# Kernel tuning notes

Measured on AMD Instinct MI355X. Metric: run time of the kernel, lower is better.

Reference implementation:

```python
import jax, jax.numpy as jnp
import numpy as np

N_NODES = 100000
N_EDGES = 1600000
NUM_FEATURES = 32
EDGE_DIM = 8
GAT_DIM = 16
HEADS = 4
HID = GAT_DIM * HEADS  # 64
OUT_DIM = 2
NUM_GRAPHS = 64
NEG_SLOPE = 0.2


def setup_inputs() -> dict:
    key = jax.random.key(0)
    ks = jax.random.split(key, 24)
    g = lambda k, shp, fan: jax.random.normal(k, shp, jnp.float32) * (1.0 / np.sqrt(fan))
    inp = {
        'x': jax.random.normal(ks[0], (N_NODES, NUM_FEATURES), jnp.float32),
        'edge_index': jax.random.randint(ks[1], (2, N_EDGES), 0, N_NODES, jnp.int64),
        'edge_attr': jax.random.normal(ks[2], (N_EDGES, EDGE_DIM), jnp.float32),
        'batch': jnp.sort(jax.random.randint(ks[3], (N_NODES,), 0, NUM_GRAPHS, jnp.int64)),
        # input GATConv params (PyG: lin bias-free, att_* of shape [H,C], bias [H*C])
        'W0': g(ks[4], (NUM_FEATURES, HID), NUM_FEATURES),
        'att_src0': g(ks[5], (HEADS, GAT_DIM), GAT_DIM),
        'att_dst0': g(ks[6], (HEADS, GAT_DIM), GAT_DIM),
        'We0': g(ks[7], (EDGE_DIM, HID), EDGE_DIM),
        'att_e0': g(ks[8], (HEADS, GAT_DIM), GAT_DIM),
        'b0': jnp.zeros((HID,), jnp.float32),
        # 2 hidden GATConv layers, stacked on a leading layer axis
        'Wh': g(ks[9], (2, HID, HID), HID),
        'att_src_h': g(ks[10], (2, HEADS, GAT_DIM), GAT_DIM),
        'att_dst_h': g(ks[11], (2, HEADS, GAT_DIM), GAT_DIM),
        'We_h': g(ks[12], (2, EDGE_DIM, HID), EDGE_DIM),
        'att_e_h': g(ks[13], (2, HEADS, GAT_DIM), GAT_DIM),
        'bh': jnp.zeros((2, HID), jnp.float32),
        # MLP head
        'fc1_w': g(ks[14], (HID, 2 * GAT_DIM), HID),
        'fc1_b': jnp.zeros((2 * GAT_DIM,), jnp.float32),
        'fc2_w': g(ks[15], (2 * GAT_DIM, OUT_DIM), 2 * GAT_DIM),
        'fc2_b': jnp.zeros((OUT_DIM,), jnp.float32),
    }
    return inp


def _gat_conv(x, src, dst, ea, W, a_s, a_d, We, a_e, b, n_nodes):
    # x: [N, Fin] -> out: [N, H*C]
    xp = (x @ W).reshape(n_nodes, HEADS, GAT_DIM)
    al_s = jnp.einsum('nhc,hc->nh', xp, a_s)            # per-node src logits
    al_d = jnp.einsum('nhc,hc->nh', xp, a_d)
    ep = (ea @ We).reshape(-1, HEADS, GAT_DIM)
    al_e = jnp.einsum('ehc,hc->eh', ep, a_e)
    alpha = jax.nn.leaky_relu(al_s[src] + al_d[dst] + al_e, NEG_SLOPE)  # [E,H]
    m = jax.ops.segment_max(alpha, dst, num_segments=n_nodes)
    m = jnp.where(jnp.isfinite(m), m, 0.0)              # nodes with no in-edges
    ex = jnp.exp(alpha - m[dst])
    den = jax.ops.segment_sum(ex, dst, num_segments=n_nodes)
    coef = ex / (den[dst] + 1e-16)                      # segment softmax over dst
    out = jax.ops.segment_sum(xp[src] * coef[..., None], dst, num_segments=n_nodes)
    return out.reshape(n_nodes, HID) + b


def _forward(x, edge_index, edge_attr, batch, W0, att_src0, att_dst0, We0, att_e0,
             b0, Wh, att_src_h, att_dst_h, We_h, att_e_h, bh, fc1_w, fc1_b, fc2_w, fc2_b):
    n = x.shape[0]
    src, dst = edge_index[0], edge_index[1]
    # PyG add_self_loops(fill_value='mean'): self-loop attr = mean of incoming edge attrs
    cnt = jax.ops.segment_sum(jnp.ones((src.shape[0],), x.dtype), dst, num_segments=n)
    mean_attr = jax.ops.segment_sum(edge_attr, dst, num_segments=n) / jnp.clip(cnt, 1.0)[:, None]
    loop = jnp.arange(n, dtype=src.dtype)
    src_sl = jnp.concatenate([src, loop])
    dst_sl = jnp.concatenate([dst, loop])
    ea_sl = jnp.concatenate([edge_attr, mean_attr], axis=0)

    h = _gat_conv(x, src_sl, dst_sl, ea_sl, W0, att_src0, att_dst0, We0, att_e0, b0, n)
    h = jax.nn.relu(h)
    for i in range(2):  # source has `x - F.relu(x)` (no-op): no ReLU between hidden layers
        h = _gat_conv(h, src_sl, dst_sl, ea_sl, Wh[i], att_src_h[i], att_dst_h[i],
                      We_h[i], att_e_h[i], bh[i], n)
    # global_mean_pool over graphs
    ones = jnp.ones((n,), h.dtype)
    gcnt = jax.ops.segment_sum(ones, batch, num_segments=NUM_GRAPHS)
    pooled = jax.ops.segment_sum(h, batch, num_segments=NUM_GRAPHS) / jnp.clip(gcnt, 1.0)[:, None]
    y = jax.nn.relu(pooled @ fc1_w + fc1_b)
    return y @ fc2_w + fc2_b


def reference(x, edge_index, edge_attr, batch, W0, att_src0, att_dst0, We0, att_e0,
              b0, Wh, att_src_h, att_dst_h, We_h, att_e_h, bh, fc1_w, fc1_b, fc2_w, fc2_b):
    return _forward(x, edge_index, edge_attr, batch, W0, att_src0, att_dst0, We0, att_e0,
                    b0, Wh, att_src_h, att_dst_h, We_h, att_e_h, bh, fc1_w, fc1_b, fc2_w, fc2_b)
```

## Files before the change

### kernel.cpp

```cpp
#include <hip/hip_runtime.h>
#include <hip/hip_bf16.h>
#include <hip/hip_fp16.h>

#define N_NODES 100000
#define N_EDGES 1600000
#define HID 64
#define NUM_GRAPHS 64
#define NEG_SLOPE 0.2f
#define SCAN_CHUNK 1024
#define SCAN_NB ((N_NODES + SCAN_CHUNK - 1) / SCAN_CHUNK)
#define ROW_W 8
#define XP_NODES_PER_BLK 16
#define POOL_NODES_PER_BLK 256
#define BUILD_NB (N_EDGES / 128)
#define XP0_NB (N_NODES / 16)


__global__ void hist_kernel(const int* __restrict__ ei, int* __restrict__ cnt,
                            int* __restrict__ rank) {
    int e = blockIdx.x * blockDim.x + threadIdx.x;
    if (e >= N_EDGES) return;
    rank[e] = atomicAdd(&cnt[ei[N_EDGES + e]], 1);
}

__global__ void scan_local_kernel(const int* __restrict__ cnt, int* __restrict__ row_ptr,
                                  int* __restrict__ bsum) {
    __shared__ int s[256];
    int t = threadIdx.x;
    int base = blockIdx.x * SCAN_CHUNK + t * 4;
    int v[4]; int sum = 0;
    #pragma unroll
    for (int i = 0; i < 4; ++i) {
        int idx = base + i;
        v[i] = (idx < N_NODES) ? cnt[idx] : 0;
        sum += v[i];
    }
    s[t] = sum;
    __syncthreads();
    for (int off = 1; off < 256; off <<= 1) {
        int x = (t >= off) ? s[t - off] : 0;
        __syncthreads();
        s[t] += x;
        __syncthreads();
    }
    int run = s[t] - sum;
    #pragma unroll
    for (int i = 0; i < 4; ++i) {
        int idx = base + i;
        if (idx < N_NODES) row_ptr[idx] = run;
        run += v[i];
    }
    if (t == 255) bsum[blockIdx.x] = s[255];
}

__global__ void scan_bsum_kernel(int* __restrict__ bsum) {
    int t = threadIdx.x;
    int orig = (t < SCAN_NB) ? bsum[t] : 0;
    int v = orig;
    #pragma unroll
    for (int off = 1; off < 64; off <<= 1) {
        int u = __shfl_up(v, off);
        if ((t & 63) >= off) v += u;
    }
    __shared__ int wtot;
    if (t == 63) wtot = v;
    __syncthreads();
    if (t >= 64) v += wtot;
    if (t < SCAN_NB) bsum[t] = v - orig;
}

__global__ void scan_add_kernel(int* __restrict__ row_ptr, const int* __restrict__ bsum) {
    int i = blockIdx.x * blockDim.x + threadIdx.x;
    if (i > N_NODES) return;
    if (i == N_NODES) row_ptr[i] = N_EDGES;
    else row_ptr[i] += bsum[i >> 10];
}

__global__ void weff_all_kernel(const float* __restrict__ We0, const float* __restrict__ ae0,
                                const float* __restrict__ Weh, const float* __restrict__ aeh,
                                float* __restrict__ weff) {
    int t = threadIdx.x;
    if (t >= 96) return;
    int layer = t >> 5, r = t & 31;
    int dd = r >> 2, h = r & 3;
    const float* We = (layer == 0) ? We0 : Weh + (size_t)(layer - 1) * 8 * 64;
    const float* ae = (layer == 0) ? ae0 : aeh + (size_t)(layer - 1) * 64;
    float s = 0.f;
    #pragma unroll
    for (int c = 0; c < 16; ++c) s += We[dd * 64 + h * 16 + c] * ae[h * 16 + c];
    weff[layer * 32 + dd * 4 + h] = s;
}

__global__ __launch_bounds__(256) void build_xp0_kernel(
    const int* __restrict__ ei, const float* __restrict__ ea,
    const int* __restrict__ row_ptr, const int* __restrict__ rank,
    const float* __restrict__ weff, unsigned int* __restrict__ ale_csr,
    const float* __restrict__ x, const float* __restrict__ W0,
    const float* __restrict__ a_s, const float* __restrict__ a_d,
    __half* __restrict__ xp, float* __restrict__ als, float* __restrict__ ald) {
    int b = blockIdx.x;
    int g = b / 3, r3 = b - g * 3;
    if (r3 == 2) {
        int wave = threadIdx.x >> 6, lane = threadIdx.x & 63;
        float wcol[32];
        #pragma unroll
        for (int k = 0; k < 32; ++k) wcol[k] = W0[k * 64 + lane];
        float asl = a_s[lane], adl = a_d[lane];
        int n0 = g * XP_NODES_PER_BLK + wave * 4;
        #pragma unroll 2
        for (int ni = 0; ni < 4; ++ni) {
            int n = n0 + ni;
            const float* xr = x + (size_t)n * 32;
            float a0 = 0.f, a1 = 0.f, a2 = 0.f, a3 = 0.f;
            #pragma unroll
            for (int k = 0; k < 32; k += 4) {
                float4 xv = *(const float4*)(xr + k);
                a0 += xv.x * wcol[k];     a1 += xv.y * wcol[k + 1];
                a2 += xv.z * wcol[k + 2]; a3 += xv.w * wcol[k + 3];
            }
            float acc = (a0 + a1) + (a2 + a3);
            xp[(size_t)n * 64 + lane] = __float2half(acc);
            float ps = acc * asl, pd = acc * adl;
            #pragma unroll
            for (int mk = 8; mk >= 1; mk >>= 1) {
                ps += __shfl_xor(ps, mk, 16);
                pd += __shfl_xor(pd, mk, 16);
            }
            if ((lane & 15) == 0) {
                als[(size_t)n * 4 + (lane >> 4)] = ps;
                ald[(size_t)n * 4 + (lane >> 4)] = pd;
            }
        }
        return;
    }
    int build_b = g * 2 + r3;
    int e = build_b * 128 + (threadIdx.x >> 1);
    int q = threadIdx.x & 1;
    int d = ei[N_EDGES + e];
    float4 a = *((const float4*)(ea + (size_t)e * 8) + q);
    float o0 = __shfl_xor(a.x, 1), o1 = __shfl_xor(a.y, 1);
    float o2 = __shfl_xor(a.z, 1), o3 = __shfl_xor(a.w, 1);
    float av[8];
    av[0] = q ? o0 : a.x;  av[1] = q ? o1 : a.y;
    av[2] = q ? o2 : a.z;  av[3] = q ? o3 : a.w;
    av[4] = q ? a.x : o0;  av[5] = q ? a.y : o1;
    av[6] = q ? a.z : o2;  av[7] = q ? a.w : o3;
    unsigned int w[4];
    if (q == 0) {
        float al[8];
        #pragma unroll
        for (int l = 0; l < 2; ++l) {
            #pragma unroll
            for (int h = 0; h < 4; ++h) {
                float s = 0.f;
                #pragma unroll
                for (int j = 0; j < 8; ++j) s += av[j] * weff[l * 32 + j * 4 + h];
                al[l * 4 + h] = s;
            }
        }
        __half2 p0 = __floats2half2_rn(al[0], al[1]);
        __half2 p1 = __floats2half2_rn(al[2], al[3]);
        __half2 p2 = __floats2half2_rn(al[4], al[5]);
        __half2 p3 = __floats2half2_rn(al[6], al[7]);
        w[0] = *(unsigned int*)&p0; w[1] = *(unsigned int*)&p1;
        w[2] = *(unsigned int*)&p2; w[3] = *(unsigned int*)&p3;
    } else {
        float al[4];
        #pragma unroll
        for (int h = 0; h < 4; ++h) {
            float s = 0.f;
            #pragma unroll
            for (int j = 0; j < 8; ++j) s += av[j] * weff[64 + j * 4 + h];
            al[h] = s;
        }
        __half2 p0 = __floats2half2_rn(al[0], al[1]);
        __half2 p1 = __floats2half2_rn(al[2], al[3]);
        w[0] = *(unsigned int*)&p0; w[1] = *(unsigned int*)&p1;
        w[2] = (unsigned int)ei[e];
        w[3] = 0u;
    }
    int pos = row_ptr[d] + rank[e];
    *(uint4*)(ale_csr + (size_t)pos * ROW_W + q * 4) =
        make_uint4(w[0], w[1], w[2], w[3]);
}

template <bool FUSE_XP>
__global__ __launch_bounds__(256) void gat_node_kernel(
    const int* __restrict__ row_ptr, const unsigned int* __restrict__ ale_csr,
    const float* __restrict__ als, const float* __restrict__ ald,
    const __half* __restrict__ xp, int layer,
    float* __restrict__ out, const float* __restrict__ bias, int relu_flag,
    const float* __restrict__ Wn, const float* __restrict__ asn,
    const float* __restrict__ adn, __half* __restrict__ xpn,
    float* __restrict__ alsn, float* __restrict__ aldn) {
    __shared__ float exl[4 * 256];
    __shared__ int   coll[4 * 64];
    __shared__ float hrow[4 * 64];
    int wave = threadIdx.x >> 6, lane = threadIdx.x & 63;
    int node = blockIdx.x * 4 + wave;
    if (node >= N_NODES) return;
    int start = row_ptr[node], end = row_ptr[node + 1];
    int deg = end - start;
    int wb = wave * 64, wb4 = wave * 256;
    int cq = lane & 15;
    int eg = lane >> 4;
    int hv = cq >> 2;

    float4 ad4  = *(const float4*)(ald + (size_t)node * 4);
    float4 asn4 = *(const float4*)(als + (size_t)node * 4);

    float4 acc4 = make_float4(0.f, 0.f, 0.f, 0.f);
    float csum = 0.f;
    float sm0 = 0.f, sm1 = 0.f, sm2 = 0.f, sm3 = 0.f;

    for (int base = 0; base < deg; base += 64) {
        int cnt = min(64, deg - base);
        float ex0 = 0.f, ex1 = 0.f, ex2 = 0.f, ex3 = 0.f;
        int s = 0;
        if (lane < cnt) {
            const unsigned int* row = ale_csr + (size_t)(start + base + lane) * ROW_W;
            uint2 alew = *(const uint2*)(row + 2 * layer);
            s = (int)row[6];
            float2 e01 = __half22float2(*(const __half2*)&alew.x);
            float2 e23 = __half22float2(*(const __half2*)&alew.y);
            sm0 += e01.x; sm1 += e01.y; sm2 += e23.x; sm3 += e23.y;
            float4 as4 = *(const float4*)(als + (size_t)s * 4);
            float v0 = as4.x + ad4.x + e01.x;
            float v1 = as4.y + ad4.y + e01.y;
            float v2 = as4.z + ad4.z + e23.x;
            float v3 = as4.w + ad4.w + e23.y;
            ex0 = __expf((v0 >= 0.f) ? v0 : NEG_SLOPE * v0);
            ex1 = __expf((v1 >= 0.f) ? v1 : NEG_SLOPE * v1);
            ex2 = __expf((v2 >= 0.f) ? v2 : NEG_SLOPE * v2);
            ex3 = __expf((v3 >= 0.f) ? v3 : NEG_SLOPE * v3);
        }
        *(float4*)(exl + wb4 + lane * 4) = make_float4(ex0, ex1, ex2, ex3);
        coll[wb + lane] = s;
        const float* exw = exl + wb4 + hv;
        int cntUp = (cnt + 15) & ~15;
        for (int j = eg; j < cntUp; j += 16) {
            int s0 = coll[wb + j],     s1 = coll[wb + j + 4];
            int s2 = coll[wb + j + 8], s3 = coll[wb + j + 12];
            float c0 = exw[(j) * 4],      c1 = exw[(j + 4) * 4];
            float c2 = exw[(j + 8) * 4],  c3 = exw[(j + 12) * 4];
            uint2 x0 = *(const uint2*)(xp + (size_t)s0 * 64 + cq * 4);
            uint2 x1 = *(const uint2*)(xp + (size_t)s1 * 64 + cq * 4);
            uint2 x2 = *(const uint2*)(xp + (size_t)s2 * 64 + cq * 4);
            uint2 x3 = *(const uint2*)(xp + (size_t)s3 * 64 + cq * 4);
            float2 f00 = __half22float2(*(const __half2*)&x0.x);
            float2 f01 = __half22float2(*(const __half2*)&x0.y);
            float2 f10 = __half22float2(*(const __half2*)&x1.x);
            float2 f11 = __half22float2(*(const __half2*)&x1.y);
            float2 f20 = __half22float2(*(const __half2*)&x2.x);
            float2 f21 = __half22float2(*(const __half2*)&x2.y);
            float2 f30 = __half22float2(*(const __half2*)&x3.x);
            float2 f31 = __half22float2(*(const __half2*)&x3.y);
            acc4.x += c0 * f00.x + c1 * f10.x + c2 * f20.x + c3 * f30.x;
            acc4.y += c0 * f00.y + c1 * f10.y + c2 * f20.y + c3 * f30.y;
            acc4.z += c0 * f01.x + c1 * f11.x + c2 * f21.x + c3 * f31.x;
            acc4.w += c0 * f01.y + c1 * f11.y + c2 * f21.y + c3 * f31.y;
            csum   += c0 + c1 + c2 + c3;
        }
    }
    #pragma unroll
    for (int mk = 1; mk < 64; mk <<= 1) {
        sm0 += __shfl_xor(sm0, mk);
        sm1 += __shfl_xor(sm1, mk);
        sm2 += __shfl_xor(sm2, mk);
        sm3 += __shfl_xor(sm3, mk);
    }
    float minv = 1.f / (float)max(deg, 1);
    float sv0 = asn4.x + ad4.x + sm0 * minv;
    float sv1 = asn4.y + ad4.y + sm1 * minv;
    float sv2 = asn4.z + ad4.z + sm2 * minv;
    float sv3 = asn4.w + ad4.w + sm3 * minv;
    float exs0 = __expf((sv0 >= 0.f) ? sv0 : NEG_SLOPE * sv0);
    float exs1 = __expf((sv1 >= 0.f) ? sv1 : NEG_SLOPE * sv1);
    float exs2 = __expf((sv2 >= 0.f) ? sv2 : NEG_SLOPE * sv2);
    float exs3 = __expf((sv3 >= 0.f) ? sv3 : NEG_SLOPE * sv3);
    float exsl = (hv < 2) ? ((hv == 0) ? exs0 : exs1)
                          : ((hv == 2) ? exs2 : exs3);
    if (eg == 0) {
        uint2 xn = *(const uint2*)(xp + (size_t)node * 64 + cq * 4);
        float2 g0 = __half22float2(*(const __half2*)&xn.x);
        float2 g1 = __half22float2(*(const __half2*)&xn.y);
        acc4.x += exsl * g0.x;
        acc4.y += exsl * g0.y;
        acc4.z += exsl * g1.x;
        acc4.w += exsl * g1.y;
        csum   += exsl;
    }
    #pragma unroll
    for (int mk = 16; mk < 64; mk <<= 1) {
        acc4.x += __shfl_xor(acc4.x, mk);
        acc4.y += __shfl_xor(acc4.y, mk);
        acc4.z += __shfl_xor(acc4.z, mk);
        acc4.w += __shfl_xor(acc4.w, mk);
        csum   += __shfl_xor(csum, mk);
    }
    float inv = 1.f / (csum + 1e-16f);
    float4 b4 = *(const float4*)(bias + cq * 4);
    float4 v;
    v.x = acc4.x * inv + b4.x;
    v.y = acc4.y * inv + b4.y;
    v.z = acc4.z * inv + b4.z;
    v.w = acc4.w * inv + b4.w;
    if (relu_flag) {
        v.x = fmaxf(v.x, 0.f); v.y = fmaxf(v.y, 0.f);
        v.z = fmaxf(v.z, 0.f); v.w = fmaxf(v.w, 0.f);
    }
    if (!FUSE_XP) {
        if (eg == 0)
            *(float4*)(out + (size_t)node * 64 + cq * 4) = v;
    } else {
        if (eg == 0) *(float4*)(hrow + wb + cq * 4) = v;
        float acc = 0.f;
        #pragma unroll
        for (int k0 = 0; k0 < 64; k0 += 8) {
            float wv[8];
            #pragma unroll
            for (int j = 0; j < 8; ++j) wv[j] = Wn[(k0 + j) * 64 + lane];
            #pragma unroll
            for (int j = 0; j < 8; ++j) acc += hrow[wb + k0 + j] * wv[j];
        }
        xpn[(size_t)node * 64 + lane] = __float2half(acc);
        float ps = acc * asn[lane], pd = acc * adn[lane];
        #pragma unroll
        for (int mk = 8; mk >= 1; mk >>= 1) {
            ps += __shfl_xor(ps, mk, 16);
            pd += __shfl_xor(pd, mk, 16);
        }
        if ((lane & 15) == 0) {
            alsn[(size_t)node * 4 + (lane >> 4)] = ps;
            aldn[(size_t)node * 4 + (lane >> 4)] = pd;
        }
    }
}

__global__ void pool_kernel(const float* __restrict__ h, const int* __restrict__ batch,
                            float* __restrict__ pooled) {
    int base = blockIdx.x * POOL_NODES_PER_BLK;
    int tid = threadIdx.x;
    int c = tid & 63, r = tid >> 6;
    float acc = 0.f;
    int curg = -1;
    for (int i = r; i < POOL_NODES_PER_BLK; i += 4) {
        int n = base + i;
        if (n >= N_NODES) break;
        int g = batch[n];
        if (g != curg) {
            if (curg >= 0) atomicAdd(&pooled[curg * 64 + c], acc);
            curg = g; acc = 0.f;
        }
        acc += h[(size_t)n * 64 + c];
    }
    if (curg >= 0) atomicAdd(&pooled[curg * 64 + c], acc);
}

__global__ void mlp_kernel(const float* __restrict__ pooled, const int* __restrict__ batch,
                           const float* __restrict__ w1, const float* __restrict__ b1,
                           const float* __restrict__ w2, const float* __restrict__ b2,
                           float* __restrict__ y) {
    int g = blockIdx.x, t = threadIdx.x;
    __shared__ float p[64], f1[32];
    __shared__ float invc_s;
    if (t == 0) {
        int lo = 0, hi = N_NODES;
        while (lo < hi) { int mid = (lo + hi) >> 1; if (batch[mid] < g) lo = mid + 1; else hi = mid; }
        int start = lo;
        hi = N_NODES;
        while (lo < hi) { int mid = (lo + hi) >> 1; if (batch[mid] < g + 1) lo = mid + 1; else hi = mid; }
        invc_s = 1.f / fmaxf((float)(lo - start), 1.f);
    }
    __syncthreads();
    p[t] = pooled[g * 64 + t] * invc_s;
    __syncthreads();
    if (t < 32) {
        float a = b1[t];
        #pragma unroll
        for (int k = 0; k < 64; ++k) a += p[k] * w1[k * 32 + t];
        f1[t] = fmaxf(a, 0.f);
    }
    __syncthreads();
    if (t < 2) {
        float a = b2[t];
        #pragma unroll
        for (int k = 0; k < 32; ++k) a += f1[k] * w2[k * 2 + t];
        y[g * 2 + t] = a;
    }
}

extern "C" void kernel_launch(void* const* d_in, const int* in_sizes, int n_in,
                              void* d_out, int out_size, void* d_ws, size_t ws_size,
                              hipStream_t stream) {
    const float* x    = (const float*)d_in[0];
    const int*   ei   = (const int*)d_in[1];
    const float* ea   = (const float*)d_in[2];
    const int*   batch= (const int*)d_in[3];
    const float* W0   = (const float*)d_in[4];
    const float* as0  = (const float*)d_in[5];
    const float* ad0  = (const float*)d_in[6];
    const float* We0  = (const float*)d_in[7];
    const float* ae0  = (const float*)d_in[8];
    const float* b0   = (const float*)d_in[9];
    const float* Wh   = (const float*)d_in[10];
    const float* ash  = (const float*)d_in[11];
    const float* adh  = (const float*)d_in[12];
    const float* Weh  = (const float*)d_in[13];
    const float* aeh  = (const float*)d_in[14];
    const float* bh   = (const float*)d_in[15];
    const float* w1   = (const float*)d_in[16];
    const float* b1   = (const float*)d_in[17];
    const float* w2   = (const float*)d_in[18];
    const float* b2   = (const float*)d_in[19];
    float* out = (float*)d_out;

    char* wsb = (char*)d_ws;
    size_t off = 0;
    auto alloc = [&](size_t bytes) { char* p = wsb + off; off += (bytes + 255) & ~(size_t)255; return p; };
    int*          row_ptr = (int*)alloc((size_t)(N_NODES + 1) * 4);
    unsigned int* ale_csr = (unsigned int*)alloc((size_t)N_EDGES * ROW_W * 4);
    float*        als0_b  = (float*)alloc((size_t)N_NODES * 4 * 4);
    float*        ald0_b  = (float*)alloc((size_t)N_NODES * 4 * 4);
    float*        als1_b  = (float*)alloc((size_t)N_NODES * 4 * 4);
    float*        ald1_b  = (float*)alloc((size_t)N_NODES * 4 * 4);
    float*        weff    = (float*)alloc(3 * 32 * 4);
    float*        pooled  = (float*)alloc((size_t)NUM_GRAPHS * 64 * 4);
    __half*       xpb0    = (__half*)alloc((size_t)N_NODES * 64 * 2);
    __half*       xpb1    = (__half*)alloc((size_t)N_NODES * 64 * 2);
    float*        bufB    = (float*)alloc((size_t)N_NODES * 64 * 4);
    int* cnt  = (int*)bufB;
    int* bsum = cnt + N_NODES;
    int* rank = bsum + ((SCAN_NB + 63) & ~63);

    weff_all_kernel<<<1, 128, 0, stream>>>(We0, ae0, Weh, aeh, weff);
    hipMemsetAsync(cnt, 0, (size_t)N_NODES * 4, stream);
    hist_kernel<<<(N_EDGES + 255) / 256, 256, 0, stream>>>(ei, cnt, rank);
    scan_local_kernel<<<SCAN_NB, 256, 0, stream>>>(cnt, row_ptr, bsum);
    scan_bsum_kernel<<<1, 128, 0, stream>>>(bsum);
    scan_add_kernel<<<(N_NODES + 256) / 256, 256, 0, stream>>>(row_ptr, bsum);
    build_xp0_kernel<<<BUILD_NB + XP0_NB, 256, 0, stream>>>(
        ei, ea, row_ptr, rank, weff, ale_csr,
        x, W0, as0, ad0, xpb0, als0_b, ald0_b);

    int gat_grid = (N_NODES + 3) / 4;
    gat_node_kernel<true><<<gat_grid, 256, 0, stream>>>(
        row_ptr, ale_csr, als0_b, ald0_b, xpb0, 0,
        nullptr, b0, 1,
        Wh, ash, adh, xpb1, als1_b, ald1_b);
    gat_node_kernel<true><<<gat_grid, 256, 0, stream>>>(
        row_ptr, ale_csr, als1_b, ald1_b, xpb1, 1,
        nullptr, bh, 0,
        Wh + (size_t)64 * 64, ash + 64, adh + 64, xpb0, als0_b, ald0_b);
    gat_node_kernel<false><<<gat_grid, 256, 0, stream>>>(
        row_ptr, ale_csr, als0_b, ald0_b, xpb0, 2,
        bufB, bh + 64, 0,
        nullptr, nullptr, nullptr, nullptr, nullptr, nullptr);

    hipMemsetAsync(pooled, 0, (size_t)NUM_GRAPHS * 64 * 4, stream);
    pool_kernel<<<(N_NODES + POOL_NODES_PER_BLK - 1) / POOL_NODES_PER_BLK, 256, 0, stream>>>(
        bufB, batch, pooled);
    mlp_kernel<<<NUM_GRAPHS, 64, 0, stream>>>(pooled, batch, w1, b1, w2, b2, out);
}
```

Before: 580.6 us.

## Assign one node per 16-lane group instead of one per wavefront

The GAT aggregation kernel now processes four nodes per wavefront, each handled by a 16-lane group, so a block covers 16 nodes instead of 4. This removes the cross-group shuffle reductions and the idle lanes that appeared for low-degree nodes, where a 64-edge chunk was mostly empty at an average degree of about 16. The fused next-layer projection is reworked so each lane computes outputs for four nodes with one load of each weight, reusing W across nodes. The cost is serial edge chunks of 16 per group, so high-degree nodes take longer. The grid drops the bounds check and assumes N_NODES is divisible by 16.

```diff
diff --git a/kernel.cpp b/kernel.cpp
--- a/kernel.cpp
+++ b/kernel.cpp
@@ -195,16 +195,20 @@
     float* __restrict__ alsn, float* __restrict__ aldn) {
     __shared__ float exl[4 * 256];
     __shared__ int   coll[4 * 64];
-    __shared__ float hrow[4 * 64];
+    __shared__ float hrow[4 * 256];
     int wave = threadIdx.x >> 6, lane = threadIdx.x & 63;
-    int node = blockIdx.x * 4 + wave;
-    if (node >= N_NODES) return;
-    int start = row_ptr[node], end = row_ptr[node + 1];
-    int deg = end - start;
-    int wb = wave * 64, wb4 = wave * 256;
-    int cq = lane & 15;
-    int eg = lane >> 4;
-    int hv = cq >> 2;
+    int grp = lane >> 4;
+    int cq  = lane & 15;
+    int hv  = cq >> 2;
+    int node = blockIdx.x * 16 + wave * 4 + grp;
+    int start = row_ptr[node];
+    int deg = row_ptr[node + 1] - start;
+    int cb = wave * 64 + grp * 16;
+    int eb = wave * 256 + grp * 64;
+
+    float asl2 = FUSE_XP ? asn[lane] : 0.f;
+    float adl2 = FUSE_XP ? adn[lane] : 0.f;
+    float4 b4 = *(const float4*)(bias + cq * 4);
 
     float4 ad4  = *(const float4*)(ald + (size_t)node * 4);
     float4 asn4 = *(const float4*)(als + (size_t)node * 4);
@@ -213,12 +217,12 @@
     float csum = 0.f;
     float sm0 = 0.f, sm1 = 0.f, sm2 = 0.f, sm3 = 0.f;
 
-    for (int base = 0; base < deg; base += 64) {
-        int cnt = min(64, deg - base);
+    for (int base = 0; base < deg; base += 16) {
+        int cnt = min(16, deg - base);
         float ex0 = 0.f, ex1 = 0.f, ex2 = 0.f, ex3 = 0.f;
         int s = 0;
-        if (lane < cnt) {
-            const unsigned int* row = ale_csr + (size_t)(start + base + lane) * ROW_W;
+        if (cq < cnt) {
+            const unsigned int* row = ale_csr + (size_t)(start + base + cq) * ROW_W;
             uint2 alew = *(const uint2*)(row + 2 * layer);
             s = (int)row[6];
             float2 e01 = __half22float2(*(const __half2*)&alew.x);
@@ -234,15 +238,15 @@
             ex2 = __expf((v2 >= 0.f) ? v2 : NEG_SLOPE * v2);
             ex3 = __expf((v3 >= 0.f) ? v3 : NEG_SLOPE * v3);
         }
-        *(float4*)(exl + wb4 + lane * 4) = make_float4(ex0, ex1, ex2, ex3);
-        coll[wb + lane] = s;
-        const float* exw = exl + wb4 + hv;
-        int cntUp = (cnt + 15) & ~15;
-        for (int j = eg; j < cntUp; j += 16) {
-            int s0 = coll[wb + j],     s1 = coll[wb + j + 4];
-            int s2 = coll[wb + j + 8], s3 = coll[wb + j + 12];
-            float c0 = exw[(j) * 4],      c1 = exw[(j + 4) * 4];
-            float c2 = exw[(j + 8) * 4],  c3 = exw[(j + 12) * 4];
+        *(float4*)(exl + eb + cq * 4) = make_float4(ex0, ex1, ex2, ex3);
+        coll[cb + cq] = s;
+        const float* exw = exl + eb + hv;
+        int cntUp = (cnt + 3) & ~3;
+        for (int j = 0; j < cntUp; j += 4) {
+            int s0 = coll[cb + j],     s1 = coll[cb + j + 1];
+            int s2 = coll[cb + j + 2], s3 = coll[cb + j + 3];
+            float c0 = exw[(j) * 4],     c1 = exw[(j + 1) * 4];
+            float c2 = exw[(j + 2) * 4], c3 = exw[(j + 3) * 4];
             uint2 x0 = *(const uint2*)(xp + (size_t)s0 * 64 + cq * 4);
             uint2 x1 = *(const uint2*)(xp + (size_t)s1 * 64 + cq * 4);
             uint2 x2 = *(const uint2*)(xp + (size_t)s2 * 64 + cq * 4);
@@ -263,24 +267,22 @@
         }
     }
     #pragma unroll
-    for (int mk = 1; mk < 64; mk <<= 1) {
-        sm0 += __shfl_xor(sm0, mk);
-        sm1 += __shfl_xor(sm1, mk);
-        sm2 += __shfl_xor(sm2, mk);
-        sm3 += __shfl_xor(sm3, mk);
+    for (int mk = 1; mk < 16; mk <<= 1) {
+        sm0 += __shfl_xor(sm0, mk, 16);
+        sm1 += __shfl_xor(sm1, mk, 16);
+        sm2 += __shfl_xor(sm2, mk, 16);
+        sm3 += __shfl_xor(sm3, mk, 16);
     }
     float minv = 1.f / (float)max(deg, 1);
-    float sv0 = asn4.x + ad4.x + sm0 * minv;
-    float sv1 = asn4.y + ad4.y + sm1 * minv;
-    float sv2 = asn4.z + ad4.z + sm2 * minv;
-    float sv3 = asn4.w + ad4.w + sm3 * minv;
-    float exs0 = __expf((sv0 >= 0.f) ? sv0 : NEG_SLOPE * sv0);
-    float exs1 = __expf((sv1 >= 0.f) ? sv1 : NEG_SLOPE * sv1);
-    float exs2 = __expf((sv2 >= 0.f) ? sv2 : NEG_SLOPE * sv2);
-    float exs3 = __expf((sv3 >= 0.f) ? sv3 : NEG_SLOPE * sv3);
-    float exsl = (hv < 2) ? ((hv == 0) ? exs0 : exs1)
-                          : ((hv == 2) ? exs2 : exs3);
-    if (eg == 0) {
+    float a_s_h = (hv < 2) ? ((hv == 0) ? asn4.x : asn4.y)
+                           : ((hv == 2) ? asn4.z : asn4.w);
+    float a_d_h = (hv < 2) ? ((hv == 0) ? ad4.x : ad4.y)
+                           : ((hv == 2) ? ad4.z : ad4.w);
+    float sm_h  = (hv < 2) ? ((hv == 0) ? sm0 : sm1)
+                           : ((hv == 2) ? sm2 : sm3);
+    float sv = a_s_h + a_d_h + sm_h * minv;
+    float exsl = __expf((sv >= 0.f) ? sv : NEG_SLOPE * sv);
+    {
         uint2 xn = *(const uint2*)(xp + (size_t)node * 64 + cq * 4);
         float2 g0 = __half22float2(*(const __half2*)&xn.x);
         float2 g1 = __half22float2(*(const __half2*)&xn.y);
@@ -290,16 +292,7 @@
         acc4.w += exsl * g1.y;
         csum   += exsl;
     }
-    #pragma unroll
-    for (int mk = 16; mk < 64; mk <<= 1) {
-        acc4.x += __shfl_xor(acc4.x, mk);
-        acc4.y += __shfl_xor(acc4.y, mk);
-        acc4.z += __shfl_xor(acc4.z, mk);
-        acc4.w += __shfl_xor(acc4.w, mk);
-        csum   += __shfl_xor(csum, mk);
-    }
     float inv = 1.f / (csum + 1e-16f);
-    float4 b4 = *(const float4*)(bias + cq * 4);
     float4 v;
     v.x = acc4.x * inv + b4.x;
     v.y = acc4.y * inv + b4.y;
@@ -310,29 +303,41 @@
         v.z = fmaxf(v.z, 0.f); v.w = fmaxf(v.w, 0.f);
     }
     if (!FUSE_XP) {
-        if (eg == 0)
-            *(float4*)(out + (size_t)node * 64 + cq * 4) = v;
+        *(float4*)(out + (size_t)node * 64 + cq * 4) = v;
     } else {
-        if (eg == 0) *(float4*)(hrow + wb + cq * 4) = v;
-        float acc = 0.f;
+        *(float4*)(hrow + eb + cq * 4) = v;
+        float pacc0 = 0.f, pacc1 = 0.f, pacc2 = 0.f, pacc3 = 0.f;
+        const float* hb = hrow + wave * 256;
         #pragma unroll
         for (int k0 = 0; k0 < 64; k0 += 8) {
             float wv[8];
             #pragma unroll
             for (int j = 0; j < 8; ++j) wv[j] = Wn[(k0 + j) * 64 + lane];
             #pragma unroll
-            for (int j = 0; j < 8; ++j) acc += hrow[wb + k0 + j] * wv[j];
-        }
-        xpn[(size_t)node * 64 + lane] = __float2half(acc);
-        float ps = acc * asn[lane], pd = acc * adn[lane];
-        #pragma unroll
-        for (int mk = 8; mk >= 1; mk >>= 1) {
-            ps += __shfl_xor(ps, mk, 16);
-            pd += __shfl_xor(pd, mk, 16);
-        }
-        if ((lane & 15) == 0) {
-            alsn[(size_t)node * 4 + (lane >> 4)] = ps;
-            aldn[(size_t)node * 4 + (lane >> 4)] = pd;
+            for (int j = 0; j < 8; ++j) {
+                float w = wv[j];
+                pacc0 += hb[k0 + j]       * w;
+                pacc1 += hb[64 + k0 + j]  * w;
+                pacc2 += hb[128 + k0 + j] * w;
+                pacc3 += hb[192 + k0 + j] * w;
+            }
+        }
+        int nodeBase = blockIdx.x * 16 + wave * 4;
+        float pa[4] = {pacc0, pacc1, pacc2, pacc3};
+        #pragma unroll
+        for (int g2 = 0; g2 < 4; ++g2) {
+            float acc = pa[g2];
+            xpn[(size_t)(nodeBase + g2) * 64 + lane] = __float2half(acc);
+            float ps = acc * asl2, pd = acc * adl2;
+            #pragma unroll
+            for (int mk = 8; mk >= 1; mk >>= 1) {
+                ps += __shfl_xor(ps, mk, 16);
+                pd += __shfl_xor(pd, mk, 16);
+            }
+            if ((lane & 15) == 0) {
+                alsn[(size_t)(nodeBase + g2) * 4 + (lane >> 4)] = ps;
+                aldn[(size_t)(nodeBase + g2) * 4 + (lane >> 4)] = pd;
+            }
         }
     }
 }
@@ -443,7 +448,7 @@
         ei, ea, row_ptr, rank, weff, ale_csr,
         x, W0, as0, ad0, xpb0, als0_b, ald0_b);
 
-    int gat_grid = (N_NODES + 3) / 4;
+    int gat_grid = N_NODES / 16;
     gat_node_kernel<true><<<gat_grid, 256, 0, stream>>>(
         row_ptr, ale_csr, als0_b, ald0_b, xpb0, 0,
         nullptr, b0, 1,
```

Measured after the change: 729.9 us. 1.26x slower.
